# Performance work log

Measured on AMD Instinct MI355X. Metric: run time of the kernel, lower is better.

The kernel has to match this reference:

```python
import jax, jax.numpy as jnp
import numpy as np

N, E, NFEAT, NHID = 50000, 800000, 256, 128
EPS = 1e-5


def setup_inputs() -> dict:
    key = jax.random.key(0)
    ks = jax.random.split(key, 12)
    s = 0.05
    return {
        "x": jax.random.normal(ks[0], (N, NFEAT), jnp.float32),
        "adj": jax.random.randint(ks[1], (2, E), 0, N, jnp.int32),
        "features": jax.random.uniform(ks[2], (E,), jnp.float32),
        "W_in": jax.random.normal(ks[3], (NHID, NFEAT), jnp.float32) * s,
        "b_in": jnp.zeros((NHID,), jnp.float32),
        "W1_rel": jax.random.normal(ks[4], (NHID, NHID), jnp.float32) * s,
        "b1_rel": jnp.zeros((NHID,), jnp.float32),
        "W1_root": jax.random.normal(ks[5], (NHID, NHID), jnp.float32) * s,
        "W2_rel": jax.random.normal(ks[6], (NHID, NHID), jnp.float32) * s,
        "b2_rel": jnp.zeros((NHID,), jnp.float32),
        "W2_root": jax.random.normal(ks[7], (NHID, NHID), jnp.float32) * s,
        "gamma": jnp.ones((NHID,), jnp.float32),
        "beta": jnp.zeros((NHID,), jnp.float32),
    }


def _graph_conv(h, src, dst, ew, W_rel, b_rel, W_root):
    # torch_geometric GraphConv (aggr='add'):
    #   out_i = W_rel @ (sum_{j->i} e_ji * h_j) + b_rel + W_root @ h_i
    msg = h[src] * ew[:, None]                       # [E, NHID] gather
    agg = jax.ops.segment_sum(msg, dst, num_segments=N)  # [N, NHID] scatter-add
    return agg @ W_rel.T + b_rel + h @ W_root.T


def _batch_norm(h, gamma, beta):
    mu = h.mean(axis=0)
    var = h.var(axis=0)
    return (h - mu) * jax.lax.rsqrt(var + EPS) * gamma + beta


def reference(x, adj, features, W_in, b_in, W1_rel, b1_rel, W1_root,
              W2_rel, b2_rel, W2_root, gamma, beta):
    src, dst = adj[0], adj[1]
    h = jax.nn.relu(x @ W_in.T + b_in)               # linear_in + relu (dropout=identity in eval)
    h = _graph_conv(h, src, dst, features, W1_rel, b1_rel, W1_root)
    h = jax.nn.relu(_batch_norm(h, gamma, beta))     # batch1 + relu
    h = _graph_conv(h, src, dst, features, W2_rel, b2_rel, W2_root)
    return _batch_norm(h, gamma, beta)               # batch1 reused (per source)
```

## Files before the change

### kernel.cpp

```cpp
#include <hip/hip_runtime.h>
#include <hip/hip_bf16.h>

#define NNODES 50000
#define NEDGES 800000
#define NF 256
#define NH 128
#define BN_EPS 1e-5f
#define MTILES (NNODES / 16)
#define GEMM_BLOCKS 512
#define NBUCKETS 196
#define BCAP 4608
#define SCAT_BLOCKS ((NEDGES + 2047) / 2048)

typedef __attribute__((ext_vector_type(8))) __bf16 bf16x8;
typedef __attribute__((ext_vector_type(4))) float floatx4;

__device__ __forceinline__ __hip_bfloat16 f2bf(float f) { return __float2bfloat16(f); }
__device__ __forceinline__ float bits2f(unsigned short b) {
    union { unsigned u; float f; } u; u.u = ((unsigned)b) << 16; return u.f;
}

__device__ __forceinline__ bf16x8 cvt8(const float* __restrict__ p) {
    floatx4 a0 = *(const floatx4*)p;
    floatx4 a1 = *(const floatx4*)(p + 4);
    bf16x8 r;
    r[0] = (__bf16)a0[0]; r[1] = (__bf16)a0[1]; r[2] = (__bf16)a0[2]; r[3] = (__bf16)a0[3];
    r[4] = (__bf16)a1[0]; r[5] = (__bf16)a1[1]; r[6] = (__bf16)a1[2]; r[7] = (__bf16)a1[3];
    return r;
}

__global__ __launch_bounds__(256) void convert_w_kernel(
    const float* __restrict__ W_in, const float* __restrict__ W1r,
    const float* __restrict__ W1o, const float* __restrict__ W2r,
    const float* __restrict__ W2o, __hip_bfloat16* __restrict__ wbf,
    int* __restrict__ gcursor, float* __restrict__ st1, float* __restrict__ st2)
{
    const int i = blockIdx.x * 256 + threadIdx.x;
    if (blockIdx.x == 0 && threadIdx.x < NBUCKETS)
        gcursor[threadIdx.x] = threadIdx.x * BCAP;
    if (blockIdx.x == 1) { st1[threadIdx.x] = 0.f; st2[threadIdx.x] = 0.f; }
    const float* src; int off;
    if (i < 32768)      { src = W_in; off = i; }
    else if (i < 49152) { src = W1r;  off = i - 32768; }
    else if (i < 65536) { src = W1o;  off = i - 49152; }
    else if (i < 81920) { src = W2r;  off = i - 65536; }
    else                { src = W2o;  off = i - 81920; }
    wbf[i] = f2bf(src[off]);
}

__global__ __launch_bounds__(256) void bucket_scatter_kernel(
    const int* __restrict__ adj, const float* __restrict__ ew,
    int* __restrict__ gcursor, uint2* __restrict__ pairbuf,
    unsigned char* __restrict__ nodebuf)
{
    __shared__ int cnt[NBUCKETS];
    __shared__ int base[NBUCKETS];
    const int tid = threadIdx.x;
    if (tid < NBUCKETS) cnt[tid] = 0;
    __syncthreads();
    const int e0 = blockIdx.x * 2048;
    #pragma unroll
    for (int i = 0; i < 8; ++i) {
        const int e = e0 + i * 256 + tid;
        if (e < NEDGES) atomicAdd(&cnt[adj[NEDGES + e] >> 8], 1);
    }
    __syncthreads();
    if (tid < NBUCKETS) {
        base[tid] = atomicAdd(&gcursor[tid], cnt[tid]);
        cnt[tid] = 0;
    }
    __syncthreads();
    #pragma unroll
    for (int i = 0; i < 8; ++i) {
        const int e = e0 + i * 256 + tid;
        if (e >= NEDGES) continue;
        const int dst = adj[NEDGES + e];
        const int b = dst >> 8;
        const int off = atomicAdd(&cnt[b], 1);
        const int slot = base[b] + off;
        if (slot < (b + 1) * BCAP) {
            pairbuf[slot] = make_uint2((unsigned)adj[e], __float_as_uint(ew[e]));
            nodebuf[slot] = (unsigned char)(dst & 255);
        }
    }
}

__global__ __launch_bounds__(256) void bucket_sort_kernel(
    const int* __restrict__ gcursor, const uint2* __restrict__ pairbuf,
    const unsigned char* __restrict__ nodebuf, uint2* __restrict__ sorted,
    int* __restrict__ rowptr, int* __restrict__ rowend)
{
    const int b = blockIdx.x;
    const int tid = threadIdx.x;
    const int capbase = b * BCAP;
    int n = gcursor[b] - capbase;
    if (n > BCAP) n = BCAP;

    __shared__ int cnt[256];
    __shared__ int s[256];
    cnt[tid] = 0;
    __syncthreads();
    for (int j = tid; j < n; j += 256)
        atomicAdd(&cnt[nodebuf[capbase + j]], 1);
    __syncthreads();
    const int v = cnt[tid];
    s[tid] = v;
    __syncthreads();
    for (int off = 1; off < 256; off <<= 1) {
        const int t = (tid >= off) ? s[tid - off] : 0;
        __syncthreads();
        s[tid] += t;
        __syncthreads();
    }
    const int excl = s[tid] - v;
    const int node = b * 256 + tid;
    if (node < NNODES) {
        rowptr[node] = capbase + excl;
        rowend[node] = capbase + excl + v;
    }
    cnt[tid] = excl;
    __syncthreads();
    for (int j = tid; j < n; j += 256) {
        const int nd = nodebuf[capbase + j];
        const int pos = atomicAdd(&cnt[nd], 1);
        sorted[capbase + pos] = pairbuf[capbase + j];
    }
}

__global__ __launch_bounds__(256, 2) void gemm_in_kernel(
    const float* __restrict__ X, const __hip_bfloat16* __restrict__ W,
    const float* __restrict__ bias, __hip_bfloat16* __restrict__ out)
{
    const int waveG = blockIdx.x * 4 + (threadIdx.x >> 6);
    const int lane = threadIdx.x & 63;
    const int half = waveG & 1;
    const int ar = lane & 15;
    const int q  = lane >> 4;

    bf16x8 bw[4][8];
    float bv[4];
    #pragma unroll
    for (int t = 0; t < 4; ++t) {
        const int row = half * 64 + t * 16 + ar;
        bv[t] = bias[row];
        #pragma unroll
        for (int k = 0; k < 8; ++k)
            bw[t][k] = *(const bf16x8*)(W + (size_t)row * NF + k * 32 + q * 8);
    }

    for (int strip = waveG >> 1; strip < MTILES; strip += GEMM_BLOCKS * 2) {
        const int m0 = strip << 4;
        floatx4 acc[4] = {};
        #pragma unroll
        for (int k = 0; k < 8; ++k) {
            const bf16x8 a = cvt8(X + (size_t)(m0 + ar) * NF + k * 32 + q * 8);
            #pragma unroll
            for (int t = 0; t < 4; ++t)
                acc[t] = __builtin_amdgcn_mfma_f32_16x16x32_bf16(a, bw[t][k], acc[t], 0, 0, 0);
        }
        #pragma unroll
        for (int t = 0; t < 4; ++t) {
            const int col = half * 64 + t * 16 + ar;
            #pragma unroll
            for (int r = 0; r < 4; ++r) {
                const float v = fmaxf(acc[t][r] + bv[t], 0.f);
                out[(size_t)(m0 + q * 4 + r) * NH + col] = f2bf(v);
            }
        }
    }
}

__global__ __launch_bounds__(256) void gather_kernel(
    const uint2* __restrict__ sorted, const int* __restrict__ rowptr,
    const int* __restrict__ rowend,
    const __hip_bfloat16* __restrict__ h, __hip_bfloat16* __restrict__ agg)
{
    const int node = blockIdx.x * 4 + (threadIdx.x >> 6);
    if (node >= NNODES) return;
    const int lane = threadIdx.x & 63;
    const int beg = rowptr[node];
    const int end = rowend[node];
    const unsigned short* hb = (const unsigned short*)h;

    float a0[8] = {}, a1[8] = {};

    int j = beg;
    if ((j & 1) && j < end) {
        const uint2 ev = sorted[j++];
        const float w = __uint_as_float(ev.y);
        const unsigned raw = *(const unsigned*)(hb + (size_t)ev.x * NH + lane * 2);
        a0[0] += w * bits2f((unsigned short)(raw & 0xffffu));
        a1[0] += w * bits2f((unsigned short)(raw >> 16));
    }
    for (; j + 8 <= end; j += 8) {
        const uint4 e01 = *(const uint4*)(sorted + j);
        const uint4 e23 = *(const uint4*)(sorted + j + 2);
        const uint4 e45 = *(const uint4*)(sorted + j + 4);
        const uint4 e67 = *(const uint4*)(sorted + j + 6);
        const unsigned r0 = *(const unsigned*)(hb + (size_t)e01.x * NH + lane * 2);
        const unsigned r1 = *(const unsigned*)(hb + (size_t)e01.z * NH + lane * 2);
        const unsigned r2 = *(const unsigned*)(hb + (size_t)e23.x * NH + lane * 2);
        const unsigned r3 = *(const unsigned*)(hb + (size_t)e23.z * NH + lane * 2);
        const unsigned r4 = *(const unsigned*)(hb + (size_t)e45.x * NH + lane * 2);
        const unsigned r5 = *(const unsigned*)(hb + (size_t)e45.z * NH + lane * 2);
        const unsigned r6 = *(const unsigned*)(hb + (size_t)e67.x * NH + lane * 2);
        const unsigned r7 = *(const unsigned*)(hb + (size_t)e67.z * NH + lane * 2);
        const float w0 = __uint_as_float(e01.y), w1 = __uint_as_float(e01.w);
        const float w2 = __uint_as_float(e23.y), w3 = __uint_as_float(e23.w);
        const float w4 = __uint_as_float(e45.y), w5 = __uint_as_float(e45.w);
        const float w6 = __uint_as_float(e67.y), w7 = __uint_as_float(e67.w);
        a0[0] += w0 * bits2f((unsigned short)(r0 & 0xffffu));
        a1[0] += w0 * bits2f((unsigned short)(r0 >> 16));
        a0[1] += w1 * bits2f((unsigned short)(r1 & 0xffffu));
        a1[1] += w1 * bits2f((unsigned short)(r1 >> 16));
        a0[2] += w2 * bits2f((unsigned short)(r2 & 0xffffu));
        a1[2] += w2 * bits2f((unsigned short)(r2 >> 16));
        a0[3] += w3 * bits2f((unsigned short)(r3 & 0xffffu));
        a1[3] += w3 * bits2f((unsigned short)(r3 >> 16));
        a0[4] += w4 * bits2f((unsigned short)(r4 & 0xffffu));
        a1[4] += w4 * bits2f((unsigned short)(r4 >> 16));
        a0[5] += w5 * bits2f((unsigned short)(r5 & 0xffffu));
        a1[5] += w5 * bits2f((unsigned short)(r5 >> 16));
        a0[6] += w6 * bits2f((unsigned short)(r6 & 0xffffu));
        a1[6] += w6 * bits2f((unsigned short)(r6 >> 16));
        a0[7] += w7 * bits2f((unsigned short)(r7 & 0xffffu));
        a1[7] += w7 * bits2f((unsigned short)(r7 >> 16));
    }
    for (; j + 2 <= end; j += 2) {
        const uint4 e01 = *(const uint4*)(sorted + j);
        const unsigned r0 = *(const unsigned*)(hb + (size_t)e01.x * NH + lane * 2);
        const unsigned r1 = *(const unsigned*)(hb + (size_t)e01.z * NH + lane * 2);
        const float w0 = __uint_as_float(e01.y), w1 = __uint_as_float(e01.w);
        a0[0] += w0 * bits2f((unsigned short)(r0 & 0xffffu));
        a1[0] += w0 * bits2f((unsigned short)(r0 >> 16));
        a0[1] += w1 * bits2f((unsigned short)(r1 & 0xffffu));
        a1[1] += w1 * bits2f((unsigned short)(r1 >> 16));
    }
    if (j < end) {
        const uint2 ev = sorted[j];
        const float w = __uint_as_float(ev.y);
        const unsigned raw = *(const unsigned*)(hb + (size_t)ev.x * NH + lane * 2);
        a0[0] += w * bits2f((unsigned short)(raw & 0xffffu));
        a1[0] += w * bits2f((unsigned short)(raw >> 16));
    }
    const float f0 = ((a0[0] + a0[1]) + (a0[2] + a0[3])) + ((a0[4] + a0[5]) + (a0[6] + a0[7]));
    const float f1 = ((a1[0] + a1[1]) + (a1[2] + a1[3])) + ((a1[4] + a1[5]) + (a1[6] + a1[7]));
    unsigned o = ((unsigned)__bfloat16_as_ushort(f2bf(f1)) << 16) |
                 (unsigned)__bfloat16_as_ushort(f2bf(f0));
    *(unsigned*)((unsigned short*)agg + (size_t)node * NH + lane * 2) = o;
}

__global__ __launch_bounds__(256, 2) void gemm_conv_kernel(
    const __hip_bfloat16* __restrict__ agg, const __hip_bfloat16* __restrict__ h,
    const __hip_bfloat16* __restrict__ Wrel, const __hip_bfloat16* __restrict__ Wroot,
    const float* __restrict__ bias, float* __restrict__ out,
    float* __restrict__ stats)
{
    const int waveG = blockIdx.x * 4 + (threadIdx.x >> 6);
    const int lane = threadIdx.x & 63;
    const int half = waveG & 1;
    const int ar = lane & 15;
    const int q  = lane >> 4;

    bf16x8 brel[4][4], brt[4][4];
    float bv[4];
    #pragma unroll
    for (int t = 0; t < 4; ++t) {
        const int row = half * 64 + t * 16 + ar;
        bv[t] = bias[row];
        #pragma unroll
        for (int k = 0; k < 4; ++k) {
            brel[t][k] = *(const bf16x8*)(Wrel + (size_t)row * NH + k * 32 + q * 8);
            brt[t][k]  = *(const bf16x8*)(Wroot + (size_t)row * NH + k * 32 + q * 8);
        }
    }

    float s1[4] = {}, s2[4] = {};

    for (int strip = waveG >> 1; strip < MTILES; strip += GEMM_BLOCKS * 2) {
        const int m0 = strip << 4;
        floatx4 acc[4] = {};
        #pragma unroll
        for (int k = 0; k < 4; ++k) {
            const bf16x8 a = *(const bf16x8*)(agg + (size_t)(m0 + ar) * NH + k * 32 + q * 8);
            #pragma unroll
            for (int t = 0; t < 4; ++t)
                acc[t] = __builtin_amdgcn_mfma_f32_16x16x32_bf16(a, brel[t][k], acc[t], 0, 0, 0);
        }
        #pragma unroll
        for (int k = 0; k < 4; ++k) {
            const bf16x8 a = *(const bf16x8*)(h + (size_t)(m0 + ar) * NH + k * 32 + q * 8);
            #pragma unroll
            for (int t = 0; t < 4; ++t)
                acc[t] = __builtin_amdgcn_mfma_f32_16x16x32_bf16(a, brt[t][k], acc[t], 0, 0, 0);
        }
        #pragma unroll
        for (int t = 0; t < 4; ++t) {
            const int col = half * 64 + t * 16 + ar;
            #pragma unroll
            for (int r = 0; r < 4; ++r) {
                const float v = acc[t][r] + bv[t];
                out[(size_t)(m0 + q * 4 + r) * NH + col] = v;
                s1[t] += v; s2[t] += v * v;
            }
        }
    }

    __shared__ float sst[256];
    sst[threadIdx.x] = 0.f;
    __syncthreads();
    #pragma unroll
    for (int t = 0; t < 4; ++t) {
        float a = s1[t], b = s2[t];
        a += __shfl_xor(a, 16, 64); a += __shfl_xor(a, 32, 64);
        b += __shfl_xor(b, 16, 64); b += __shfl_xor(b, 32, 64);
        if (q == 0) {
            const int col = half * 64 + t * 16 + ar;
            atomicAdd(&sst[col], a);
            atomicAdd(&sst[128 + col], b);
        }
    }
    __syncthreads();
    unsafeAtomicAdd(&stats[threadIdx.x], sst[threadIdx.x]);
}

__global__ __launch_bounds__(256) void bn_relu_bf16_kernel(
    const float* __restrict__ t, const float* __restrict__ stats,
    const float* __restrict__ gamma, const float* __restrict__ beta,
    __hip_bfloat16* __restrict__ out)
{
    const size_t i = (size_t)blockIdx.x * blockDim.x + threadIdx.x;
    const int c = (int)(i & (NH - 1));
    const float inv_n = 1.0f / (float)NNODES;
    const float mu = stats[c] * inv_n;
    const float var = stats[128 + c] * inv_n - mu * mu;
    const float rs = rsqrtf(var + BN_EPS);
    float v = (t[i] - mu) * rs * gamma[c] + beta[c];
    out[i] = f2bf(fmaxf(v, 0.f));
}

__global__ __launch_bounds__(256) void bn_f32_kernel(
    const float* __restrict__ t, const float* __restrict__ stats,
    const float* __restrict__ gamma, const float* __restrict__ beta,
    float* __restrict__ out)
{
    const size_t i = (size_t)blockIdx.x * blockDim.x + threadIdx.x;
    const int c = (int)(i & (NH - 1));
    const float inv_n = 1.0f / (float)NNODES;
    const float mu = stats[c] * inv_n;
    const float var = stats[128 + c] * inv_n - mu * mu;
    const float rs = rsqrtf(var + BN_EPS);
    out[i] = (t[i] - mu) * rs * gamma[c] + beta[c];
}


extern "C" void kernel_launch(void* const* d_in, const int* in_sizes, int n_in,
                              void* d_out, int out_size, void* d_ws, size_t ws_size,
                              hipStream_t stream)
{
    const float* x    = (const float*)d_in[0];
    const int*   adj  = (const int*)d_in[1];
    const float* ew   = (const float*)d_in[2];
    const float* W_in = (const float*)d_in[3];
    const float* b_in = (const float*)d_in[4];
    const float* W1r  = (const float*)d_in[5];
    const float* b1   = (const float*)d_in[6];
    const float* W1o  = (const float*)d_in[7];
    const float* W2r  = (const float*)d_in[8];
    const float* b2   = (const float*)d_in[9];
    const float* W2o  = (const float*)d_in[10];
    const float* gmm  = (const float*)d_in[11];
    const float* bta  = (const float*)d_in[12];
    float* out = (float*)d_out;
    float* t   = (float*)d_out;

    char* ws = (char*)d_ws;
    __hip_bfloat16* h0  = (__hip_bfloat16*)ws; ws += (size_t)NNODES * NH * 2;
    __hip_bfloat16* h1  = (__hip_bfloat16*)ws; ws += (size_t)NNODES * NH * 2;
    __hip_bfloat16* agg = (__hip_bfloat16*)ws; ws += (size_t)NNODES * NH * 2;
    uint2*          sorted  = (uint2*)ws;      ws += (size_t)NBUCKETS * BCAP * 8;
    uint2*          pairbuf = (uint2*)ws;      ws += (size_t)NBUCKETS * BCAP * 8;
    unsigned char*  nodebuf = (unsigned char*)ws; ws += (size_t)NBUCKETS * BCAP;
    int*            rowptr  = (int*)ws;        ws += NNODES * 4;
    int*            rowend  = (int*)ws;        ws += NNODES * 4;
    int*            gcursor = (int*)ws;        ws += ((NBUCKETS + 3) & ~3) * 4;
    __hip_bfloat16* wbf     = (__hip_bfloat16*)ws; ws += 98304 * 2;
    float*          st1     = (float*)ws;      ws += 256 * 4;
    float*          st2     = (float*)ws;      ws += 256 * 4;

    const __hip_bfloat16* Wb_in = wbf;
    const __hip_bfloat16* Wb1r  = wbf + 32768;
    const __hip_bfloat16* Wb1o  = wbf + 49152;
    const __hip_bfloat16* Wb2r  = wbf + 65536;
    const __hip_bfloat16* Wb2o  = wbf + 81920;

    const int node_blocks = (NNODES + 3) / 4;
    const int bn_blocks   = (NNODES * NH) / 256;

    convert_w_kernel<<<98304 / 256, 256, 0, stream>>>(W_in, W1r, W1o, W2r, W2o,
                                                      wbf, gcursor, st1, st2);
    bucket_scatter_kernel<<<SCAT_BLOCKS, 256, 0, stream>>>(adj, ew, gcursor, pairbuf, nodebuf);
    bucket_sort_kernel<<<NBUCKETS, 256, 0, stream>>>(gcursor, pairbuf, nodebuf,
                                                     sorted, rowptr, rowend);

    gemm_in_kernel<<<GEMM_BLOCKS, 256, 0, stream>>>(x, Wb_in, b_in, h0);
    gather_kernel<<<node_blocks, 256, 0, stream>>>(sorted, rowptr, rowend, h0, agg);
    gemm_conv_kernel<<<GEMM_BLOCKS, 256, 0, stream>>>(agg, h0, Wb1r, Wb1o, b1, t, st1);
    bn_relu_bf16_kernel<<<bn_blocks, 256, 0, stream>>>(t, st1, gmm, bta, h1);

    gather_kernel<<<node_blocks, 256, 0, stream>>>(sorted, rowptr, rowend, h1, agg);
    gemm_conv_kernel<<<GEMM_BLOCKS, 256, 0, stream>>>(agg, h1, Wb2r, Wb2o, b2, t, st2);
    bn_f32_kernel<<<bn_blocks, 256, 0, stream>>>(t, st2, gmm, bta, out);
}
```

Baseline: 329.8 us.

## Fuse GraphConv GEMM with batch-norm via cooperative grid sync; merge prep kernels

```diff
diff --git a/kernel.cpp b/kernel.cpp
--- a/kernel.cpp
+++ b/kernel.cpp
@@ -1,5 +1,8 @@
 #include <hip/hip_runtime.h>
 #include <hip/hip_bf16.h>
+#include <hip/hip_cooperative_groups.h>
+
+namespace cg = cooperative_groups;
 
 #define NNODES 50000
 #define NEDGES 800000
@@ -11,6 +14,7 @@
 #define NBUCKETS 196
 #define BCAP 4608
 #define SCAT_BLOCKS ((NEDGES + 2047) / 2048)
+#define CONV_BLOCKS (98304 / 256)
 
 typedef __attribute__((ext_vector_type(8))) __bf16 bf16x8;
 typedef __attribute__((ext_vector_type(4))) float floatx4;
@@ -29,33 +33,30 @@
     return r;
 }
 
-__global__ __launch_bounds__(256) void convert_w_kernel(
+__global__ __launch_bounds__(256) void prep_kernel(
+    const int* __restrict__ adj, const float* __restrict__ ew,
+    int* __restrict__ gcursor, uint2* __restrict__ pairbuf,
+    unsigned char* __restrict__ nodebuf,
     const float* __restrict__ W_in, const float* __restrict__ W1r,
     const float* __restrict__ W1o, const float* __restrict__ W2r,
-    const float* __restrict__ W2o, __hip_bfloat16* __restrict__ wbf,
-    int* __restrict__ gcursor, float* __restrict__ st1, float* __restrict__ st2)
-{
-    const int i = blockIdx.x * 256 + threadIdx.x;
-    if (blockIdx.x == 0 && threadIdx.x < NBUCKETS)
-        gcursor[threadIdx.x] = threadIdx.x * BCAP;
-    if (blockIdx.x == 1) { st1[threadIdx.x] = 0.f; st2[threadIdx.x] = 0.f; }
-    const float* src; int off;
-    if (i < 32768)      { src = W_in; off = i; }
-    else if (i < 49152) { src = W1r;  off = i - 32768; }
-    else if (i < 65536) { src = W1o;  off = i - 49152; }
-    else if (i < 81920) { src = W2r;  off = i - 65536; }
-    else                { src = W2o;  off = i - 81920; }
-    wbf[i] = f2bf(src[off]);
-}
-
-__global__ __launch_bounds__(256) void bucket_scatter_kernel(
-    const int* __restrict__ adj, const float* __restrict__ ew,
-    int* __restrict__ gcursor, uint2* __restrict__ pairbuf,
-    unsigned char* __restrict__ nodebuf)
+    const float* __restrict__ W2o, __hip_bfloat16* __restrict__ wbf)
 {
     __shared__ int cnt[NBUCKETS];
     __shared__ int base[NBUCKETS];
     const int tid = threadIdx.x;
+
+    if (blockIdx.x >= SCAT_BLOCKS) {
+        const int i = (blockIdx.x - SCAT_BLOCKS) * 256 + tid;
+        const float* src; int off;
+        if (i < 32768)      { src = W_in; off = i; }
+        else if (i < 49152) { src = W1r;  off = i - 32768; }
+        else if (i < 65536) { src = W1o;  off = i - 49152; }
+        else if (i < 81920) { src = W2r;  off = i - 65536; }
+        else                { src = W2o;  off = i - 81920; }
+        wbf[i] = f2bf(src[off]);
+        return;
+    }
+
     if (tid < NBUCKETS) cnt[tid] = 0;
     __syncthreads();
     const int e0 = blockIdx.x * 2048;
@@ -66,7 +67,7 @@
     }
     __syncthreads();
     if (tid < NBUCKETS) {
-        base[tid] = atomicAdd(&gcursor[tid], cnt[tid]);
+        base[tid] = tid * BCAP + atomicAdd(&gcursor[tid], cnt[tid]);
         cnt[tid] = 0;
     }
     __syncthreads();
@@ -93,7 +94,7 @@
     const int b = blockIdx.x;
     const int tid = threadIdx.x;
     const int capbase = b * BCAP;
-    int n = gcursor[b] - capbase;
+    int n = gcursor[b];
     if (n > BCAP) n = BCAP;
 
     __shared__ int cnt[256];
@@ -250,6 +251,121 @@
     *(unsigned*)((unsigned short*)agg + (size_t)node * NH + lane * 2) = o;
 }
 
+template<int LAYER>
+__global__ __launch_bounds__(256, 2) void gemm_conv_bn_kernel(
+    const __hip_bfloat16* __restrict__ agg, const __hip_bfloat16* __restrict__ h,
+    const __hip_bfloat16* __restrict__ Wrel, const __hip_bfloat16* __restrict__ Wroot,
+    const float* __restrict__ bias, const float* __restrict__ gamma,
+    const float* __restrict__ beta, float* __restrict__ stats,
+    void* __restrict__ outv)
+{
+    const int waveG = blockIdx.x * 4 + (threadIdx.x >> 6);
+    const int lane = threadIdx.x & 63;
+    const int half = waveG & 1;
+    const int ar = lane & 15;
+    const int q  = lane >> 4;
+
+    bf16x8 brel[4][4], brt[4][4];
+    float bv[4], gv[4], btv[4];
+    #pragma unroll
+    for (int t = 0; t < 4; ++t) {
+        const int row = half * 64 + t * 16 + ar;
+        bv[t]  = bias[row];
+        gv[t]  = gamma[row];
+        btv[t] = beta[row];
+        #pragma unroll
+        for (int k = 0; k < 4; ++k) {
+            brel[t][k] = *(const bf16x8*)(Wrel + (size_t)row * NH + k * 32 + q * 8);
+            brt[t][k]  = *(const bf16x8*)(Wroot + (size_t)row * NH + k * 32 + q * 8);
+        }
+    }
+
+    float s1[4] = {}, s2[4] = {};
+    floatx4 accS[4][4] = {};
+    const int base = waveG >> 1;
+
+    #pragma unroll
+    for (int s = 0; s < 4; ++s) {
+        const int strip = base + s * (GEMM_BLOCKS * 2);
+        if (strip >= MTILES) continue;
+        const int m0 = strip << 4;
+        #pragma unroll
+        for (int k = 0; k < 4; ++k) {
+            const bf16x8 a = *(const bf16x8*)(agg + (size_t)(m0 + ar) * NH + k * 32 + q * 8);
+            #pragma unroll
+            for (int t = 0; t < 4; ++t)
+                accS[s][t] = __builtin_amdgcn_mfma_f32_16x16x32_bf16(a, brel[t][k], accS[s][t], 0, 0, 0);
+        }
+        #pragma unroll
+        for (int k = 0; k < 4; ++k) {
+            const bf16x8 a = *(const bf16x8*)(h + (size_t)(m0 + ar) * NH + k * 32 + q * 8);
+            #pragma unroll
+            for (int t = 0; t < 4; ++t)
+                accS[s][t] = __builtin_amdgcn_mfma_f32_16x16x32_bf16(a, brt[t][k], accS[s][t], 0, 0, 0);
+        }
+        #pragma unroll
+        for (int t = 0; t < 4; ++t) {
+            #pragma unroll
+            for (int r = 0; r < 4; ++r) {
+                const float v = accS[s][t][r] + bv[t];
+                s1[t] += v; s2[t] += v * v;
+            }
+        }
+    }
+
+    __shared__ float sst[256];
+    sst[threadIdx.x] = 0.f;
+    __syncthreads();
+    #pragma unroll
+    for (int t = 0; t < 4; ++t) {
+        float a = s1[t], b = s2[t];
+        a += __shfl_xor(a, 16, 64); a += __shfl_xor(a, 32, 64);
+        b += __shfl_xor(b, 16, 64); b += __shfl_xor(b, 32, 64);
+        if (q == 0) {
+            const int col = half * 64 + t * 16 + ar;
+            atomicAdd(&sst[col], a);
+            atomicAdd(&sst[128 + col], b);
+        }
+    }
+    __syncthreads();
+    unsafeAtomicAdd(&stats[threadIdx.x], sst[threadIdx.x]);
+
+    cg::this_grid().sync();
+
+    const float inv_n = 1.0f / (float)NNODES;
+    float mu[4], rsg[4];
+    #pragma unroll
+    for (int t = 0; t < 4; ++t) {
+        const int col = half * 64 + t * 16 + ar;
+        const float m = stats[col] * inv_n;
+        const float var = stats[128 + col] * inv_n - m * m;
+        mu[t]  = m;
+        rsg[t] = rsqrtf(var + BN_EPS) * gv[t];
+    }
+
+    #pragma unroll
+    for (int s = 0; s < 4; ++s) {
+        const int strip = base + s * (GEMM_BLOCKS * 2);
+        if (strip >= MTILES) continue;
+        const int m0 = strip << 4;
+        #pragma unroll
+        for (int t = 0; t < 4; ++t) {
+            const int col = half * 64 + t * 16 + ar;
+            #pragma unroll
+            for (int r = 0; r < 4; ++r) {
+                float v = accS[s][t][r] + bv[t];
+                v = (v - mu[t]) * rsg[t] + btv[t];
+                if (LAYER == 0) {
+                    ((__hip_bfloat16*)outv)[(size_t)(m0 + q * 4 + r) * NH + col] =
+                        f2bf(fmaxf(v, 0.f));
+                } else {
+                    ((float*)outv)[(size_t)(m0 + q * 4 + r) * NH + col] = v;
+                }
+            }
+        }
+    }
+}
+
 __global__ __launch_bounds__(256, 2) void gemm_conv_kernel(
     const __hip_bfloat16* __restrict__ agg, const __hip_bfloat16* __restrict__ h,
     const __hip_bfloat16* __restrict__ Wrel, const __hip_bfloat16* __restrict__ Wroot,
@@ -372,7 +488,6 @@
     const float* gmm  = (const float*)d_in[11];
     const float* bta  = (const float*)d_in[12];
     float* out = (float*)d_out;
-    float* t   = (float*)d_out;
 
     char* ws = (char*)d_ws;
     __hip_bfloat16* h0  = (__hip_bfloat16*)ws; ws += (size_t)NNODES * NH * 2;
@@ -383,10 +498,10 @@
     unsigned char*  nodebuf = (unsigned char*)ws; ws += (size_t)NBUCKETS * BCAP;
     int*            rowptr  = (int*)ws;        ws += NNODES * 4;
     int*            rowend  = (int*)ws;        ws += NNODES * 4;
-    int*            gcursor = (int*)ws;        ws += ((NBUCKETS + 3) & ~3) * 4;
-    __hip_bfloat16* wbf     = (__hip_bfloat16*)ws; ws += 98304 * 2;
+    int*            gcursor = (int*)ws;        ws += 256 * 4;
     float*          st1     = (float*)ws;      ws += 256 * 4;
     float*          st2     = (float*)ws;      ws += 256 * 4;
+    __hip_bfloat16* wbf     = (__hip_bfloat16*)ws; ws += 98304 * 2;
 
     const __hip_bfloat16* Wb_in = wbf;
     const __hip_bfloat16* Wb1r  = wbf + 32768;
@@ -397,18 +512,40 @@
     const int node_blocks = (NNODES + 3) / 4;
     const int bn_blocks   = (NNODES * NH) / 256;
 
-    convert_w_kernel<<<98304 / 256, 256, 0, stream>>>(W_in, W1r, W1o, W2r, W2o,
-                                                      wbf, gcursor, st1, st2);
-    bucket_scatter_kernel<<<SCAT_BLOCKS, 256, 0, stream>>>(adj, ew, gcursor, pairbuf, nodebuf);
+    hipMemsetAsync(gcursor, 0, 3 * 256 * 4, stream);
+    prep_kernel<<<SCAT_BLOCKS + CONV_BLOCKS, 256, 0, stream>>>(
+        adj, ew, gcursor, pairbuf, nodebuf, W_in, W1r, W1o, W2r, W2o, wbf);
     bucket_sort_kernel<<<NBUCKETS, 256, 0, stream>>>(gcursor, pairbuf, nodebuf,
                                                      sorted, rowptr, rowend);
 
     gemm_in_kernel<<<GEMM_BLOCKS, 256, 0, stream>>>(x, Wb_in, b_in, h0);
     gather_kernel<<<node_blocks, 256, 0, stream>>>(sorted, rowptr, rowend, h0, agg);
-    gemm_conv_kernel<<<GEMM_BLOCKS, 256, 0, stream>>>(agg, h0, Wb1r, Wb1o, b1, t, st1);
-    bn_relu_bf16_kernel<<<bn_blocks, 256, 0, stream>>>(t, st1, gmm, bta, h1);
+    {
+        const __hip_bfloat16* a_ = agg; const __hip_bfloat16* h_ = h0;
+        const __hip_bfloat16* wr_ = Wb1r; const __hip_bfloat16* wo_ = Wb1o;
+        const float* b_ = b1; const float* g_ = gmm; const float* bt_ = bta;
+        float* s_ = st1; void* o_ = (void*)h1;
+        void* args[9] = { &a_, &h_, &wr_, &wo_, &b_, &g_, &bt_, &s_, &o_ };
+        hipError_t err = hipLaunchCooperativeKernel(
+            gemm_conv_bn_kernel<0>, dim3(GEMM_BLOCKS), dim3(256), args, 0, stream);
+        if (err != hipSuccess) {
+            gemm_conv_kernel<<<GEMM_BLOCKS, 256, 0, stream>>>(agg, h0, Wb1r, Wb1o, b1, out, st1);
+            bn_relu_bf16_kernel<<<bn_blocks, 256, 0, stream>>>(out, st1, gmm, bta, h1);
+        }
+    }
 
     gather_kernel<<<node_blocks, 256, 0, stream>>>(sorted, rowptr, rowend, h1, agg);
-    gemm_conv_kernel<<<GEMM_BLOCKS, 256, 0, stream>>>(agg, h1, Wb2r, Wb2o, b2, t, st2);
-    bn_f32_kernel<<<bn_blocks, 256, 0, stream>>>(t, st2, gmm, bta, out);
-}
+    {
+        const __hip_bfloat16* a_ = agg; const __hip_bfloat16* h_ = h1;
+        const __hip_bfloat16* wr_ = Wb2r; const __hip_bfloat16* wo_ = Wb2o;
+        const float* b_ = b2; const float* g_ = gmm; const float* bt_ = bta;
+        float* s_ = st2; void* o_ = (void*)out;
+        void* args[9] = { &a_, &h_, &wr_, &wo_, &b_, &g_, &bt_, &s_, &o_ };
+        hipError_t err = hipLaunchCooperativeKernel(
+            gemm_conv_bn_kernel<1>, dim3(GEMM_BLOCKS), dim3(256), args, 0, stream);
+        if (err != hipSuccess) {
+            gemm_conv_kernel<<<GEMM_BLOCKS, 256, 0, stream>>>(agg, h1, Wb2r, Wb2o, b2, out, st2);
+            bn_f32_kernel<<<bn_blocks, 256, 0, stream>>>(out, st2, gmm, bta, out);
+        }
+    }
+}
```

Measured after the change: 382.6 us. 16.0% more time.

## Stage conv weights in LDS and merge weight conversion into edge bucketing

Applied to the files above, without the earlier changes.

```diff
diff --git a/kernel.cpp b/kernel.cpp
--- a/kernel.cpp
+++ b/kernel.cpp
@@ -8,9 +8,11 @@
 #define BN_EPS 1e-5f
 #define MTILES (NNODES / 16)
 #define GEMM_BLOCKS 512
+#define CONV_BLOCKS2 512
 #define NBUCKETS 196
 #define BCAP 4608
 #define SCAT_BLOCKS ((NEDGES + 2047) / 2048)
+#define WCONV_BLOCKS (98304 / 256)
 
 typedef __attribute__((ext_vector_type(8))) __bf16 bf16x8;
 typedef __attribute__((ext_vector_type(4))) float floatx4;
@@ -29,33 +31,30 @@
     return r;
 }
 
-__global__ __launch_bounds__(256) void convert_w_kernel(
+__global__ __launch_bounds__(256) void prep_kernel(
+    const int* __restrict__ adj, const float* __restrict__ ew,
+    int* __restrict__ gcursor, uint2* __restrict__ pairbuf,
+    unsigned char* __restrict__ nodebuf,
     const float* __restrict__ W_in, const float* __restrict__ W1r,
     const float* __restrict__ W1o, const float* __restrict__ W2r,
-    const float* __restrict__ W2o, __hip_bfloat16* __restrict__ wbf,
-    int* __restrict__ gcursor, float* __restrict__ st1, float* __restrict__ st2)
-{
-    const int i = blockIdx.x * 256 + threadIdx.x;
-    if (blockIdx.x == 0 && threadIdx.x < NBUCKETS)
-        gcursor[threadIdx.x] = threadIdx.x * BCAP;
-    if (blockIdx.x == 1) { st1[threadIdx.x] = 0.f; st2[threadIdx.x] = 0.f; }
-    const float* src; int off;
-    if (i < 32768)      { src = W_in; off = i; }
-    else if (i < 49152) { src = W1r;  off = i - 32768; }
-    else if (i < 65536) { src = W1o;  off = i - 49152; }
-    else if (i < 81920) { src = W2r;  off = i - 65536; }
-    else                { src = W2o;  off = i - 81920; }
-    wbf[i] = f2bf(src[off]);
-}
-
-__global__ __launch_bounds__(256) void bucket_scatter_kernel(
-    const int* __restrict__ adj, const float* __restrict__ ew,
-    int* __restrict__ gcursor, uint2* __restrict__ pairbuf,
-    unsigned char* __restrict__ nodebuf)
+    const float* __restrict__ W2o, __hip_bfloat16* __restrict__ wbf)
 {
     __shared__ int cnt[NBUCKETS];
     __shared__ int base[NBUCKETS];
     const int tid = threadIdx.x;
+
+    if (blockIdx.x >= SCAT_BLOCKS) {
+        const int i = (blockIdx.x - SCAT_BLOCKS) * 256 + tid;
+        const float* src; int off;
+        if (i < 32768)      { src = W_in; off = i; }
+        else if (i < 49152) { src = W1r;  off = i - 32768; }
+        else if (i < 65536) { src = W1o;  off = i - 49152; }
+        else if (i < 81920) { src = W2r;  off = i - 65536; }
+        else                { src = W2o;  off = i - 81920; }
+        wbf[i] = f2bf(src[off]);
+        return;
+    }
+
     if (tid < NBUCKETS) cnt[tid] = 0;
     __syncthreads();
     const int e0 = blockIdx.x * 2048;
@@ -66,7 +65,7 @@
     }
     __syncthreads();
     if (tid < NBUCKETS) {
-        base[tid] = atomicAdd(&gcursor[tid], cnt[tid]);
+        base[tid] = tid * BCAP + atomicAdd(&gcursor[tid], cnt[tid]);
         cnt[tid] = 0;
     }
     __syncthreads();
@@ -93,7 +92,7 @@
     const int b = blockIdx.x;
     const int tid = threadIdx.x;
     const int capbase = b * BCAP;
-    int n = gcursor[b] - capbase;
+    int n = gcursor[b];
     if (n > BCAP) n = BCAP;
 
     __shared__ int cnt[256];
@@ -250,78 +249,78 @@
     *(unsigned*)((unsigned short*)agg + (size_t)node * NH + lane * 2) = o;
 }
 
-__global__ __launch_bounds__(256, 2) void gemm_conv_kernel(
+#define LROW 528
+
+__global__ __launch_bounds__(512, 4) void gemm_conv_kernel(
     const __hip_bfloat16* __restrict__ agg, const __hip_bfloat16* __restrict__ h,
     const __hip_bfloat16* __restrict__ Wrel, const __hip_bfloat16* __restrict__ Wroot,
     const float* __restrict__ bias, float* __restrict__ out,
     float* __restrict__ stats)
 {
-    const int waveG = blockIdx.x * 4 + (threadIdx.x >> 6);
-    const int lane = threadIdx.x & 63;
-    const int half = waveG & 1;
+    __shared__ char wlds[128 * LROW];
+    __shared__ float sst[256];
+    const int tid = threadIdx.x;
+    if (tid < 256) sst[tid] = 0.f;
+
+    {
+        const int r = tid >> 2, part = tid & 3;
+        const __hip_bfloat16* src = (part < 2 ? Wrel : Wroot) + (size_t)r * NH + (part & 1) * 64;
+        char* dst = wlds + r * LROW + part * 128;
+        #pragma unroll
+        for (int j = 0; j < 8; ++j)
+            *(bf16x8*)(dst + j * 16) = *(const bf16x8*)(src + j * 8);
+    }
+    __syncthreads();
+
+    const int lane = tid & 63;
     const int ar = lane & 15;
     const int q  = lane >> 4;
-
-    bf16x8 brel[4][4], brt[4][4];
-    float bv[4];
-    #pragma unroll
-    for (int t = 0; t < 4; ++t) {
-        const int row = half * 64 + t * 16 + ar;
-        bv[t] = bias[row];
-        #pragma unroll
-        for (int k = 0; k < 4; ++k) {
-            brel[t][k] = *(const bf16x8*)(Wrel + (size_t)row * NH + k * 32 + q * 8);
-            brt[t][k]  = *(const bf16x8*)(Wroot + (size_t)row * NH + k * 32 + q * 8);
-        }
-    }
-
-    float s1[4] = {}, s2[4] = {};
-
-    for (int strip = waveG >> 1; strip < MTILES; strip += GEMM_BLOCKS * 2) {
+    const int strip = blockIdx.x * 8 + (tid >> 6);
+
+    if (strip < MTILES) {
         const int m0 = strip << 4;
-        floatx4 acc[4] = {};
-        #pragma unroll
-        for (int k = 0; k < 4; ++k) {
-            const bf16x8 a = *(const bf16x8*)(agg + (size_t)(m0 + ar) * NH + k * 32 + q * 8);
+        float bv[8];
+        #pragma unroll
+        for (int t = 0; t < 8; ++t) bv[t] = bias[t * 16 + ar];
+
+        floatx4 acc[8] = {};
+        const char* wl = wlds + ar * LROW + q * 16;
+        #pragma unroll
+        for (int kk = 0; kk < 4; ++kk) {
+            const bf16x8 a = *(const bf16x8*)(agg + (size_t)(m0 + ar) * NH + kk * 32 + q * 8);
             #pragma unroll
-            for (int t = 0; t < 4; ++t)
-                acc[t] = __builtin_amdgcn_mfma_f32_16x16x32_bf16(a, brel[t][k], acc[t], 0, 0, 0);
-        }
-        #pragma unroll
-        for (int k = 0; k < 4; ++k) {
-            const bf16x8 a = *(const bf16x8*)(h + (size_t)(m0 + ar) * NH + k * 32 + q * 8);
+            for (int t = 0; t < 8; ++t)
+                acc[t] = __builtin_amdgcn_mfma_f32_16x16x32_bf16(
+                    a, *(const bf16x8*)(wl + t * (16 * LROW) + kk * 64), acc[t], 0, 0, 0);
+        }
+        #pragma unroll
+        for (int kk = 0; kk < 4; ++kk) {
+            const bf16x8 a = *(const bf16x8*)(h + (size_t)(m0 + ar) * NH + kk * 32 + q * 8);
             #pragma unroll
-            for (int t = 0; t < 4; ++t)
-                acc[t] = __builtin_amdgcn_mfma_f32_16x16x32_bf16(a, brt[t][k], acc[t], 0, 0, 0);
-        }
-        #pragma unroll
-        for (int t = 0; t < 4; ++t) {
-            const int col = half * 64 + t * 16 + ar;
+            for (int t = 0; t < 8; ++t)
+                acc[t] = __builtin_amdgcn_mfma_f32_16x16x32_bf16(
+                    a, *(const bf16x8*)(wl + t * (16 * LROW) + 256 + kk * 64), acc[t], 0, 0, 0);
+        }
+
+        #pragma unroll
+        for (int t = 0; t < 8; ++t) {
+            float s1 = 0.f, s2 = 0.f;
             #pragma unroll
             for (int r = 0; r < 4; ++r) {
                 const float v = acc[t][r] + bv[t];
-                out[(size_t)(m0 + q * 4 + r) * NH + col] = v;
-                s1[t] += v; s2[t] += v * v;
+                out[(size_t)(m0 + q * 4 + r) * NH + t * 16 + ar] = v;
+                s1 += v; s2 += v * v;
             }
-        }
-    }
-
-    __shared__ float sst[256];
-    sst[threadIdx.x] = 0.f;
-    __syncthreads();
-    #pragma unroll
-    for (int t = 0; t < 4; ++t) {
-        float a = s1[t], b = s2[t];
-        a += __shfl_xor(a, 16, 64); a += __shfl_xor(a, 32, 64);
-        b += __shfl_xor(b, 16, 64); b += __shfl_xor(b, 32, 64);
-        if (q == 0) {
-            const int col = half * 64 + t * 16 + ar;
-            atomicAdd(&sst[col], a);
-            atomicAdd(&sst[128 + col], b);
-        }
-    }
-    __syncthreads();
-    unsafeAtomicAdd(&stats[threadIdx.x], sst[threadIdx.x]);
+            s1 += __shfl_xor(s1, 16, 64); s1 += __shfl_xor(s1, 32, 64);
+            s2 += __shfl_xor(s2, 16, 64); s2 += __shfl_xor(s2, 32, 64);
+            if (q == 0) {
+                atomicAdd(&sst[t * 16 + ar], s1);
+                atomicAdd(&sst[128 + t * 16 + ar], s2);
+            }
+        }
+    }
+    __syncthreads();
+    if (tid < 256) unsafeAtomicAdd(&stats[tid], sst[tid]);
 }
 
 __global__ __launch_bounds__(256) void bn_relu_bf16_kernel(
@@ -383,10 +382,10 @@
     unsigned char*  nodebuf = (unsigned char*)ws; ws += (size_t)NBUCKETS * BCAP;
     int*            rowptr  = (int*)ws;        ws += NNODES * 4;
     int*            rowend  = (int*)ws;        ws += NNODES * 4;
-    int*            gcursor = (int*)ws;        ws += ((NBUCKETS + 3) & ~3) * 4;
-    __hip_bfloat16* wbf     = (__hip_bfloat16*)ws; ws += 98304 * 2;
+    int*            gcursor = (int*)ws;        ws += 256 * 4;
     float*          st1     = (float*)ws;      ws += 256 * 4;
     float*          st2     = (float*)ws;      ws += 256 * 4;
+    __hip_bfloat16* wbf     = (__hip_bfloat16*)ws; ws += 98304 * 2;
 
     const __hip_bfloat16* Wb_in = wbf;
     const __hip_bfloat16* Wb1r  = wbf + 32768;
@@ -397,18 +396,18 @@
     const int node_blocks = (NNODES + 3) / 4;
     const int bn_blocks   = (NNODES * NH) / 256;
 
-    convert_w_kernel<<<98304 / 256, 256, 0, stream>>>(W_in, W1r, W1o, W2r, W2o,
-                                                      wbf, gcursor, st1, st2);
-    bucket_scatter_kernel<<<SCAT_BLOCKS, 256, 0, stream>>>(adj, ew, gcursor, pairbuf, nodebuf);
+    hipMemsetAsync(gcursor, 0, 3 * 256 * 4, stream);
+    prep_kernel<<<SCAT_BLOCKS + WCONV_BLOCKS, 256, 0, stream>>>(
+        adj, ew, gcursor, pairbuf, nodebuf, W_in, W1r, W1o, W2r, W2o, wbf);
     bucket_sort_kernel<<<NBUCKETS, 256, 0, stream>>>(gcursor, pairbuf, nodebuf,
                                                      sorted, rowptr, rowend);
 
     gemm_in_kernel<<<GEMM_BLOCKS, 256, 0, stream>>>(x, Wb_in, b_in, h0);
     gather_kernel<<<node_blocks, 256, 0, stream>>>(sorted, rowptr, rowend, h0, agg);
-    gemm_conv_kernel<<<GEMM_BLOCKS, 256, 0, stream>>>(agg, h0, Wb1r, Wb1o, b1, t, st1);
+    gemm_conv_kernel<<<CONV_BLOCKS2, 512, 0, stream>>>(agg, h0, Wb1r, Wb1o, b1, t, st1);
     bn_relu_bf16_kernel<<<bn_blocks, 256, 0, stream>>>(t, st1, gmm, bta, h1);
 
     gather_kernel<<<node_blocks, 256, 0, stream>>>(sorted, rowptr, rowend, h1, agg);
-    gemm_conv_kernel<<<GEMM_BLOCKS, 256, 0, stream>>>(agg, h1, Wb2r, Wb2o, b2, t, st2);
+    gemm_conv_kernel<<<CONV_BLOCKS2, 512, 0, stream>>>(agg, h1, Wb2r, Wb2o, b2, t, st2);
     bn_f32_kernel<<<bn_blocks, 256, 0, stream>>>(t, st2, gmm, bta, out);
 }
```

New measurement: 304.9 us. -7.6%, faster.
